# Optimization experiments

Measured on AMD Instinct MI355X. Metric: run time of the kernel, lower is better.

The kernel has to match this reference:

```python
import jax, jax.numpy as jnp
import numpy as np

# Sizes (match input_specs)
B = 50                 # number of CRN graphs in the batch
NS_PER, NR_PER = 2000, 4000
N_S, N_R = B * NS_PER, B * NR_PER   # 100k species, 200k reactions total
E = 1_000_000          # bipartite edges
D = 128                # d_model
L = 2                  # n_layers
N_TYPES, P_DIM = 16, 8
MAX_SPECIES_IDX = 2000


def setup_inputs() -> dict:
    key = jax.random.key(0)
    ks = jax.random.split(key, 12)
    inp = {
        "species_indices": jax.random.randint(ks[0], (N_S,), 0, MAX_SPECIES_IDX, dtype=jnp.int32),
        "is_external": jax.random.randint(ks[1], (N_S,), 0, 2, dtype=jnp.int32),
        "propensity_type_ids": jax.random.randint(ks[2], (N_R,), 0, N_TYPES, dtype=jnp.int32),
        "propensity_params": jax.random.normal(ks[3], (N_R, P_DIM), dtype=jnp.float32),
        "edge_species": jax.random.randint(ks[4], (E,), 0, N_S, dtype=jnp.int32),
        "edge_reaction": jax.random.randint(ks[5], (E,), 0, N_R, dtype=jnp.int32),
        # contiguous per-graph segment ids (graphs are equal-sized)
        "species_batch": jnp.repeat(jnp.arange(B, dtype=jnp.int32), NS_PER),
        "reaction_batch": jnp.repeat(jnp.arange(B, dtype=jnp.int32), NR_PER),
        # learned parameters
        "species_table": jax.random.normal(ks[6], (MAX_SPECIES_IDX, D), dtype=jnp.float32) * 0.02,
        "external_table": jax.random.normal(ks[7], (2, D), dtype=jnp.float32) * 0.02,
        "type_table": jax.random.normal(ks[8], (N_TYPES, D), dtype=jnp.float32) * 0.02,
        "W_param": jax.random.normal(ks[9], (P_DIM, D), dtype=jnp.float32) * 0.1,
        "b_param": jnp.zeros((D,), dtype=jnp.float32),
        # per-layer message-passing weights: concat([h, msg]) -> d
        "Wr": jax.random.normal(ks[10], (L, 2 * D, D), dtype=jnp.float32) * 0.05,
        "br": jnp.zeros((L, D), dtype=jnp.float32),
        "Ws": jax.random.normal(ks[11], (L, 2 * D, D), dtype=jnp.float32) * 0.05,
        "bs": jnp.zeros((L, D), dtype=jnp.float32),
    }
    return inp


def reference(species_indices, is_external, propensity_type_ids, propensity_params,
              edge_species, edge_reaction, species_batch, reaction_batch,
              species_table, external_table, type_table, W_param, b_param,
              Wr, br, Ws, bs):
    # Initial embeddings
    h_s = species_table[species_indices] + external_table[is_external]          # (N_S, D)
    h_r = type_table[propensity_type_ids] + propensity_params @ W_param + b_param  # (N_R, D)

    n_s, n_r = h_s.shape[0], h_r.shape[0]
    # Alternating bipartite sum message passing (SumMessagePassingLayer)
    for l in range(Wr.shape[0]):
        m_r = jax.ops.segment_sum(h_s[edge_species], edge_reaction, num_segments=n_r)
        h_r = jax.nn.relu(jnp.concatenate([h_r, m_r], axis=-1) @ Wr[l] + br[l])
        m_s = jax.ops.segment_sum(h_r[edge_reaction], edge_species, num_segments=n_s)
        h_s = jax.nn.relu(jnp.concatenate([h_s, m_s], axis=-1) @ Ws[l] + bs[l])

    # Segment-mean pooling per graph (index_add then divide by counts)
    pooled_s = jax.ops.segment_sum(h_s, species_batch, num_segments=B) / float(NS_PER)
    pooled_r = jax.ops.segment_sum(h_r, reaction_batch, num_segments=B) / float(NR_PER)
    context = jnp.concatenate([pooled_s, pooled_r], axis=-1)  # (B, 2D); dropout p=0 -> identity
    return context
```

## Files before the change

kernel.cpp:

```cpp
#include <hip/hip_runtime.h>
#include <stdint.h>

#define NS 100000
#define NR 200000
#define EE 1000000
#define DD 128
#define NB 50
#define NSP 2000
#define NRP 4000
#define BSH 10
#define NBR 196
#define NBS 98
#define CHUNK 8192

typedef short bf16x8 __attribute__((ext_vector_type(8)));
typedef float f32x4 __attribute__((ext_vector_type(4)));
typedef unsigned u32x4 __attribute__((ext_vector_type(4)));

__device__ __forceinline__ unsigned short f2bf(float f){
  unsigned u = __float_as_uint(f);
  u = (u + 0x7FFFu + ((u >> 16) & 1u)) >> 16;
  return (unsigned short)u;
}
__device__ __forceinline__ float bf2f(unsigned short s){
  return __uint_as_float(((unsigned)s) << 16);
}
__device__ __forceinline__ unsigned packbf(float a, float b){
  return (unsigned)f2bf(a) | ((unsigned)f2bf(b) << 16);
}
__device__ __forceinline__ float bflo(unsigned p){ return __uint_as_float(p << 16); }
__device__ __forceinline__ float bfhi(unsigned p){ return __uint_as_float(p & 0xFFFF0000u); }

__global__ void pack_w(const float* __restrict__ Wr, const float* __restrict__ Ws,
                       unsigned short* __restrict__ Wp){
  int g = blockIdx.x*256 + threadIdx.x;
  if (g >= 4*32768) return;
  int j = g & 7; int rest = g >> 3;
  int lane = rest & 63; rest >>= 6;
  int ks = rest & 7; rest >>= 3;
  int ct = rest & 7; int mat = rest >> 3;
  int k  = ks*32 + (lane >> 4)*8 + j;
  int cc = ct*16 + (lane & 15);
  const float* src = (mat < 2) ? (Wr + (size_t)mat*256*DD) : (Ws + (size_t)(mat-2)*256*DD);
  Wp[g] = f2bf(src[(size_t)k*DD + cc]);
}

__global__ __launch_bounds__(256) void init_all(const int* __restrict__ si, const int* __restrict__ ext,
        const int* __restrict__ tid, const float* __restrict__ pp,
        const float* __restrict__ st, const float* __restrict__ et, const float* __restrict__ tt,
        const float* __restrict__ Wpar, const float* __restrict__ bpar,
        unsigned short* __restrict__ hs, unsigned short* __restrict__ hr){
  int g = blockIdx.x*256 + threadIdx.x;
  int row = g >> 4, colb = (g & 15) * 8;
  if (row < NS){
    const float* a = st + (size_t)si[row]*DD + colb;
    const float* b = et + (size_t)ext[row]*DD + colb;
    float4 x0 = ((const float4*)a)[0], x1 = ((const float4*)a)[1];
    float4 y0 = ((const float4*)b)[0], y1 = ((const float4*)b)[1];
    u32x4 o;
    o.x = packbf(x0.x+y0.x, x0.y+y0.y);
    o.y = packbf(x0.z+y0.z, x0.w+y0.w);
    o.z = packbf(x1.x+y1.x, x1.y+y1.y);
    o.w = packbf(x1.z+y1.z, x1.w+y1.w);
    *(u32x4*)(hs + (size_t)row*DD + colb) = o;
  } else {
    int r = row - NS;
    const float* tb = tt + (size_t)tid[r]*DD + colb;
    float4 a0 = ((const float4*)tb)[0], a1 = ((const float4*)tb)[1];
    float4 b0 = ((const float4*)(bpar+colb))[0], b1 = ((const float4*)(bpar+colb))[1];
    a0.x += b0.x; a0.y += b0.y; a0.z += b0.z; a0.w += b0.w;
    a1.x += b1.x; a1.y += b1.y; a1.z += b1.z; a1.w += b1.w;
    const float* pr = pp + (size_t)r*8;
    float4 p0 = ((const float4*)pr)[0], p1 = ((const float4*)pr)[1];
    float w[8] = {p0.x,p0.y,p0.z,p0.w,p1.x,p1.y,p1.z,p1.w};
    #pragma unroll
    for (int p = 0; p < 8; p++){
      float4 w0 = ((const float4*)(Wpar + p*DD + colb))[0];
      float4 w1 = ((const float4*)(Wpar + p*DD + colb))[1];
      a0.x += w[p]*w0.x; a0.y += w[p]*w0.y; a0.z += w[p]*w0.z; a0.w += w[p]*w0.w;
      a1.x += w[p]*w1.x; a1.y += w[p]*w1.y; a1.z += w[p]*w1.z; a1.w += w[p]*w1.w;
    }
    u32x4 o;
    o.x = packbf(a0.x, a0.y); o.y = packbf(a0.z, a0.w);
    o.z = packbf(a1.x, a1.y); o.w = packbf(a1.z, a1.w);
    *(u32x4*)(hr + (size_t)r*DD + colb) = o;
  }
}

__global__ __launch_bounds__(256) void bucket_hist(const int* __restrict__ er, const int* __restrict__ es,
                                                   int* __restrict__ gcnt){
  __shared__ int cnt[NBR + NBS];
  int t = threadIdx.x;
  for (int j = t; j < NBR + NBS; j += 256) cnt[j] = 0;
  __syncthreads();
  long i0 = (long)blockIdx.x * 2048;
  for (int j = t; j < 2048; j += 256){
    long i = i0 + j;
    if (i < EE){
      atomicAdd(&cnt[er[i] >> BSH], 1);
      atomicAdd(&cnt[NBR + (es[i] >> BSH)], 1);
    }
  }
  __syncthreads();
  for (int j = t; j < NBR + NBS; j += 256)
    if (cnt[j]) atomicAdd(&gcnt[j], cnt[j]);
}

__global__ __launch_bounds__(256) void bucket_scan(const int* __restrict__ gcnt,
        int* __restrict__ bktOffR, int* __restrict__ bktOffS,
        int* __restrict__ gCurR, int* __restrict__ gCurS){
  __shared__ int a[256];
  int t = threadIdx.x;
  int own = (t < NBR) ? gcnt[t] : 0;
  a[t] = own; __syncthreads();
  for (int d = 1; d < 256; d <<= 1){
    int x = (t >= d) ? a[t-d] : 0;
    __syncthreads(); a[t] += x; __syncthreads();
  }
  if (t < NBR){ int v = a[t] - own; bktOffR[t] = v; gCurR[t] = v; }
  if (t == 0) bktOffR[NBR] = EE;
  __syncthreads();
  own = (t < NBS) ? gcnt[NBR + t] : 0;
  a[t] = own; __syncthreads();
  for (int d = 1; d < 256; d <<= 1){
    int x = (t >= d) ? a[t-d] : 0;
    __syncthreads(); a[t] += x; __syncthreads();
  }
  if (t < NBS){ int v = a[t] - own; bktOffS[t] = v; gCurS[t] = v; }
  if (t == 0) bktOffS[NBS] = EE;
}

__global__ __launch_bounds__(256) void bin_edges(const int* __restrict__ er, const int* __restrict__ es,
        int* __restrict__ gCurR, int* __restrict__ gCurS,
        unsigned* __restrict__ recR, unsigned* __restrict__ recS){
  __shared__ unsigned stage[CHUNK];
  __shared__ unsigned char stageb[CHUNK];
  __shared__ int cnt[256], scn[256], pref[256], gbase[256], lcur[256];
  int t = threadIdx.x;
  int side = blockIdx.y;
  const int* dest = side ? es : er;
  const int* srca = side ? er : es;
  int* gCur = side ? gCurS : gCurR;
  unsigned* rec = side ? recS : recR;
  int nbkt = side ? NBS : NBR;
  long i0 = (long)blockIdx.x * CHUNK;
  int n = (EE - i0 < CHUNK) ? (int)(EE - i0) : CHUNK;
  cnt[t] = 0;
  __syncthreads();
  for (int j = t; j < n; j += 256)
    atomicAdd(&cnt[dest[i0 + j] >> BSH], 1);
  __syncthreads();
  scn[t] = cnt[t];
  __syncthreads();
  for (int d = 1; d < 256; d <<= 1){
    int x = (t >= d) ? scn[t-d] : 0;
    __syncthreads(); scn[t] += x; __syncthreads();
  }
  pref[t] = scn[t] - cnt[t];
  lcur[t] = scn[t] - cnt[t];
  if (t < nbkt && cnt[t] > 0) gbase[t] = atomicAdd(&gCur[t], cnt[t]);
  __syncthreads();
  for (int j = t; j < n; j += 256){
    int d = dest[i0 + j];
    int s = srca[i0 + j];
    int b = d >> BSH;
    int p = atomicAdd(&lcur[b], 1);
    stage[p] = ((unsigned)(d - (b << BSH)) << 18) | (unsigned)s;
    stageb[p] = (unsigned char)b;
  }
  __syncthreads();
  for (int e = t; e < n; e += 256){
    int b = stageb[e];
    rec[gbase[b] + (e - pref[b])] = stage[e];
  }
}

__global__ __launch_bounds__(256) void build_csr(const unsigned* __restrict__ recR, const unsigned* __restrict__ recS,
        const int* __restrict__ bktOffR, const int* __restrict__ bktOffS,
        int* __restrict__ csrR, int* __restrict__ csrS,
        int* __restrict__ offsR, int* __restrict__ offsS){
  __shared__ int hist[1024], pref[1024], cur[1024], ws[256];
  int t = threadIdx.x;
  int bb = blockIdx.x;
  const unsigned* rec; const int* bktOff; int* csr; int* offs; int N;
  if (bb < NBR){ rec = recR; bktOff = bktOffR; csr = csrR; offs = offsR; N = NR; }
  else { bb -= NBR; rec = recS; bktOff = bktOffS; csr = csrS; offs = offsS; N = NS; }
  int d0 = bb << BSH;
  int base = bktOff[bb], cnt_ = bktOff[bb+1] - base;
  #pragma unroll
  for (int j = 0; j < 4; j++) hist[t*4+j] = 0;
  __syncthreads();
  for (int e = t; e < cnt_; e += 256)
    atomicAdd(&hist[rec[base + e] >> 18], 1);
  __syncthreads();
  int s = 0, h[4];
  #pragma unroll
  for (int j = 0; j < 4; j++){ h[j] = hist[t*4+j]; s += h[j]; }
  ws[t] = s;
  __syncthreads();
  for (int d = 1; d < 256; d <<= 1){
    int x = (t >= d) ? ws[t-d] : 0;
    __syncthreads(); ws[t] += x; __syncthreads();
  }
  int run = ws[t] - s;
  #pragma unroll
  for (int j = 0; j < 4; j++){ pref[t*4+j] = run; cur[t*4+j] = base + run; run += h[j]; }
  __syncthreads();
  int DPB = N - d0; if (DPB > 1024) DPB = 1024;
  #pragma unroll
  for (int j = 0; j < 4; j++){
    int i = t*4 + j;
    if (i < DPB) offs[d0 + i] = base + pref[i];
  }
  if (t == 0 && d0 + DPB == N) offs[N] = EE;
  __syncthreads();
  for (int e = t; e < cnt_; e += 256){
    unsigned r = rec[base + e];
    int pos = atomicAdd(&cur[r >> 18], 1);
    csr[pos] = (int)(r & 0x3FFFFu);
  }
}

__global__ __launch_bounds__(256) void gather(const unsigned short* __restrict__ h, const int* __restrict__ offs,
        const int* __restrict__ csr, unsigned short* __restrict__ m, int nrows){
  int gw = (blockIdx.x * 256 + threadIdx.x) >> 6;
  int lane = threadIdx.x & 63;
  int quad = lane >> 4, sub = lane & 15;
  int r = gw*4 + quad;
  if (r >= nrows) return;
  int b = offs[r], e = offs[r+1];
  float a0=0,a1=0,a2=0,a3=0,a4=0,a5=0,a6=0,a7=0;
  float c0=0,c1=0,c2=0,c3=0,c4=0,c5=0,c6=0,c7=0;
  int k = b;
  for (; k + 2 <= e; k += 2){
    int s0 = csr[k], s1 = csr[k+1];
    u32x4 p = *(const u32x4*)(h + (size_t)s0*DD + sub*8);
    u32x4 q = *(const u32x4*)(h + (size_t)s1*DD + sub*8);
    a0 += bflo(p.x); a1 += bfhi(p.x); a2 += bflo(p.y); a3 += bfhi(p.y);
    a4 += bflo(p.z); a5 += bfhi(p.z); a6 += bflo(p.w); a7 += bfhi(p.w);
    c0 += bflo(q.x); c1 += bfhi(q.x); c2 += bflo(q.y); c3 += bfhi(q.y);
    c4 += bflo(q.z); c5 += bfhi(q.z); c6 += bflo(q.w); c7 += bfhi(q.w);
  }
  if (k < e){
    u32x4 p = *(const u32x4*)(h + (size_t)csr[k]*DD + sub*8);
    a0 += bflo(p.x); a1 += bfhi(p.x); a2 += bflo(p.y); a3 += bfhi(p.y);
    a4 += bflo(p.z); a5 += bfhi(p.z); a6 += bflo(p.w); a7 += bfhi(p.w);
  }
  u32x4 o;
  o.x = packbf(a0+c0, a1+c1); o.y = packbf(a2+c2, a3+c3);
  o.z = packbf(a4+c4, a5+c5); o.w = packbf(a6+c6, a7+c7);
  *(u32x4*)(m + (size_t)r*DD + sub*8) = o;
}

__global__ __launch_bounds__(256) void relu_gemm(const unsigned short* __restrict__ H,
        const unsigned short* __restrict__ M, const unsigned short* __restrict__ Wp,
        const float* __restrict__ bias, unsigned short* __restrict__ Hout, int N)
{
  int t = threadIdx.x;
  int lane = t & 63;
  int w = t >> 6;
  int rlo = lane & 15, quad = lane >> 4;
  int ct0 = w * 2;

  bf16x8 bf[16];
  #pragma unroll
  for (int ks = 0; ks < 8; ks++){
    bf[ks*2+0] = *(const bf16x8*)(Wp + (size_t)(((ct0+0)*8 + ks)*64 + lane) * 8);
    bf[ks*2+1] = *(const bf16x8*)(Wp + (size_t)(((ct0+1)*8 + ks)*64 + lane) * 8);
  }
  float bv0 = bias[(ct0+0)*16 + rlo];
  float bv1 = bias[(ct0+1)*16 + rlo];

  int ntiles = N >> 5;
  for (int tile = blockIdx.x; tile < ntiles; tile += gridDim.x){
    int row0 = tile * 32;
    f32x4 acc[2][2];
    #pragma unroll
    for (int i = 0; i < 2; i++)
      #pragma unroll
      for (int j = 0; j < 2; j++){ f32x4 z = {0.f,0.f,0.f,0.f}; acc[i][j] = z; }

    #pragma unroll
    for (int ks = 0; ks < 8; ks++){
      const unsigned short* src = (ks < 4) ? H : M;
      int kloc = (ks & 3) * 32 + quad * 8;
      bf16x8 a0 = *(const bf16x8*)(src + (size_t)(row0 + rlo) * DD + kloc);
      bf16x8 a1 = *(const bf16x8*)(src + (size_t)(row0 + 16 + rlo) * DD + kloc);
      acc[0][0] = __builtin_amdgcn_mfma_f32_16x16x32_bf16(a0, bf[ks*2+0], acc[0][0], 0, 0, 0);
      acc[0][1] = __builtin_amdgcn_mfma_f32_16x16x32_bf16(a0, bf[ks*2+1], acc[0][1], 0, 0, 0);
      acc[1][0] = __builtin_amdgcn_mfma_f32_16x16x32_bf16(a1, bf[ks*2+0], acc[1][0], 0, 0, 0);
      acc[1][1] = __builtin_amdgcn_mfma_f32_16x16x32_bf16(a1, bf[ks*2+1], acc[1][1], 0, 0, 0);
    }

    #pragma unroll
    for (int rb = 0; rb < 2; rb++){
      #pragma unroll
      for (int i = 0; i < 4; i++){
        int row = row0 + rb*16 + quad*4 + i;
        float v0 = acc[rb][0][i] + bv0;
        float v1 = acc[rb][1][i] + bv1;
        v0 = v0 > 0.f ? v0 : 0.f;
        v1 = v1 > 0.f ? v1 : 0.f;
        Hout[(size_t)row*DD + (ct0+0)*16 + rlo] = f2bf(v0);
        Hout[(size_t)row*DD + (ct0+1)*16 + rlo] = f2bf(v1);
      }
    }
  }
}

__global__ __launch_bounds__(256) void pool(const unsigned short* __restrict__ hs,
        const unsigned short* __restrict__ hr, float* __restrict__ out){
  __shared__ float red[16][128];
  int b = blockIdx.x, part = blockIdx.y;
  int t = threadIdx.x;
  int rg = t >> 4, sub = t & 15;
  const unsigned short* src; int row0, outoff; float scale;
  if (part < 4){ src = hs; row0 = b*NSP + part*500; outoff = b*256; scale = 1.f/NSP; }
  else { src = hr; row0 = b*NRP + (part-4)*500; outoff = b*256 + 128; scale = 1.f/NRP; }
  float a0=0,a1=0,a2=0,a3=0,a4=0,a5=0,a6=0,a7=0;
  for (int r = rg; r < 500; r += 16){
    u32x4 p = *(const u32x4*)(src + (size_t)(row0+r)*DD + sub*8);
    a0 += bflo(p.x); a1 += bfhi(p.x);
    a2 += bflo(p.y); a3 += bfhi(p.y);
    a4 += bflo(p.z); a5 += bfhi(p.z);
    a6 += bflo(p.w); a7 += bfhi(p.w);
  }
  float* rr = &red[rg][sub*8];
  rr[0]=a0; rr[1]=a1; rr[2]=a2; rr[3]=a3; rr[4]=a4; rr[5]=a5; rr[6]=a6; rr[7]=a7;
  __syncthreads();
  if (t < 128){
    float s = 0.f;
    #pragma unroll
    for (int g = 0; g < 16; g++) s += red[g][t];
    atomicAdd(&out[outoff + t], s * scale);
  }
}

extern "C" void kernel_launch(void* const* d_in, const int* in_sizes, int n_in,
                              void* d_out, int out_size, void* d_ws, size_t ws_size,
                              hipStream_t stream)
{
  const int*   si   = (const int*)d_in[0];
  const int*   ext  = (const int*)d_in[1];
  const int*   tid  = (const int*)d_in[2];
  const float* pp   = (const float*)d_in[3];
  const int*   es   = (const int*)d_in[4];
  const int*   er   = (const int*)d_in[5];
  const float* st   = (const float*)d_in[8];
  const float* et   = (const float*)d_in[9];
  const float* tt   = (const float*)d_in[10];
  const float* Wpar = (const float*)d_in[11];
  const float* bpar = (const float*)d_in[12];
  const float* Wr   = (const float*)d_in[13];
  const float* br   = (const float*)d_in[14];
  const float* Ws   = (const float*)d_in[15];
  const float* bs   = (const float*)d_in[16];
  float* out = (float*)d_out;

  char* basep = (char*)d_ws; size_t off = 0;
  auto alloc = [&](size_t bytes)->char*{
    char* r = basep + off; off = (off + bytes + 255) & ~(size_t)255; return r;
  };
  unsigned short* h_s = (unsigned short*)alloc((size_t)NS*DD*2);
  unsigned short* h_r = (unsigned short*)alloc((size_t)NR*DD*2);
  unsigned short* msg = (unsigned short*)alloc((size_t)NR*DD*2);
  unsigned short* Wp  = (unsigned short*)alloc((size_t)4*32768*2);
  int* offsR = (int*)alloc((size_t)(NR+1)*4);
  int* offsS = (int*)alloc((size_t)(NS+1)*4);
  int* csrR  = (int*)alloc((size_t)EE*4);
  int* csrS  = (int*)alloc((size_t)EE*4);
  unsigned* recR = (unsigned*)alloc((size_t)EE*4);
  unsigned* recS = (unsigned*)alloc((size_t)EE*4);
  int* gcnt   = (int*)alloc(2048);
  int* bktOffR= (int*)alloc(2048);
  int* bktOffS= (int*)alloc(2048);
  int* gCurR  = (int*)alloc(2048);
  int* gCurS  = (int*)alloc(2048);

  hipMemsetAsync(gcnt, 0, 2048, stream);
  hipMemsetAsync(d_out, 0, (size_t)out_size*4, stream);

  pack_w<<<512, 256, 0, stream>>>(Wr, Ws, Wp);
  init_all<<<(NS+NR)*16/256, 256, 0, stream>>>(si, ext, tid, pp, st, et, tt, Wpar, bpar, h_s, h_r);

  bucket_hist<<<(EE + 2047)/2048, 256, 0, stream>>>(er, es, gcnt);
  bucket_scan<<<1, 256, 0, stream>>>(gcnt, bktOffR, bktOffS, gCurR, gCurS);
  bin_edges<<<dim3((EE + CHUNK - 1)/CHUNK, 2), 256, 0, stream>>>(er, es, gCurR, gCurS, recR, recS);
  build_csr<<<NBR + NBS, 256, 0, stream>>>(recR, recS, bktOffR, bktOffS, csrR, csrS, offsR, offsS);

  for (int l = 0; l < 2; l++){
    gather<<<(NR + 15)/16, 256, 0, stream>>>(h_s, offsR, csrR, msg, NR);
    relu_gemm<<<1024, 256, 0, stream>>>(h_r, msg, Wp + (size_t)l*32768, br + (size_t)l*DD, h_r, NR);
    gather<<<(NS + 15)/16, 256, 0, stream>>>(h_r, offsS, csrS, msg, NS);
    relu_gemm<<<1024, 256, 0, stream>>>(h_s, msg, Wp + (size_t)(2+l)*32768, bs + (size_t)l*DD, h_s, NS);
  }

  pool<<<dim3(NB, 12), 256, 0, stream>>>(h_s, h_r, out);
}
```

Measured before the change: 550.5 us.

## Fuse neighbor gather into ReLU GEMM per 32-row tile via shared memory

```diff
diff --git a/kernel.cpp b/kernel.cpp
--- a/kernel.cpp
+++ b/kernel.cpp
@@ -16,6 +16,7 @@
 typedef short bf16x8 __attribute__((ext_vector_type(8)));
 typedef float f32x4 __attribute__((ext_vector_type(4)));
 typedef unsigned u32x4 __attribute__((ext_vector_type(4)));
+typedef unsigned u32x2 __attribute__((ext_vector_type(2)));
 
 __device__ __forceinline__ unsigned short f2bf(float f){
   unsigned u = __float_as_uint(f);
@@ -30,6 +31,11 @@
 }
 __device__ __forceinline__ float bflo(unsigned p){ return __uint_as_float(p << 16); }
 __device__ __forceinline__ float bfhi(unsigned p){ return __uint_as_float(p & 0xFFFF0000u); }
+
+__device__ __forceinline__ void acc8(float* a, u32x4 p){
+  a[0] += bflo(p.x); a[1] += bfhi(p.x); a[2] += bflo(p.y); a[3] += bfhi(p.y);
+  a[4] += bflo(p.z); a[5] += bfhi(p.z); a[6] += bflo(p.w); a[7] += bfhi(p.w);
+}
 
 __global__ void pack_w(const float* __restrict__ Wr, const float* __restrict__ Ws,
                        unsigned short* __restrict__ Wp){
@@ -221,89 +227,122 @@
   }
 }
 
-__global__ __launch_bounds__(256) void gather(const unsigned short* __restrict__ h, const int* __restrict__ offs,
-        const int* __restrict__ csr, unsigned short* __restrict__ m, int nrows){
-  int gw = (blockIdx.x * 256 + threadIdx.x) >> 6;
-  int lane = threadIdx.x & 63;
-  int quad = lane >> 4, sub = lane & 15;
-  int r = gw*4 + quad;
-  if (r >= nrows) return;
-  int b = offs[r], e = offs[r+1];
-  float a0=0,a1=0,a2=0,a3=0,a4=0,a5=0,a6=0,a7=0;
-  float c0=0,c1=0,c2=0,c3=0,c4=0,c5=0,c6=0,c7=0;
-  int k = b;
-  for (; k + 2 <= e; k += 2){
-    int s0 = csr[k], s1 = csr[k+1];
-    u32x4 p = *(const u32x4*)(h + (size_t)s0*DD + sub*8);
-    u32x4 q = *(const u32x4*)(h + (size_t)s1*DD + sub*8);
-    a0 += bflo(p.x); a1 += bfhi(p.x); a2 += bflo(p.y); a3 += bfhi(p.y);
-    a4 += bflo(p.z); a5 += bfhi(p.z); a6 += bflo(p.w); a7 += bfhi(p.w);
-    c0 += bflo(q.x); c1 += bfhi(q.x); c2 += bflo(q.y); c3 += bfhi(q.y);
-    c4 += bflo(q.z); c5 += bfhi(q.z); c6 += bflo(q.w); c7 += bfhi(q.w);
-  }
-  if (k < e){
-    u32x4 p = *(const u32x4*)(h + (size_t)csr[k]*DD + sub*8);
-    a0 += bflo(p.x); a1 += bfhi(p.x); a2 += bflo(p.y); a3 += bfhi(p.y);
-    a4 += bflo(p.z); a5 += bfhi(p.z); a6 += bflo(p.w); a7 += bfhi(p.w);
-  }
-  u32x4 o;
-  o.x = packbf(a0+c0, a1+c1); o.y = packbf(a2+c2, a3+c3);
-  o.z = packbf(a4+c4, a5+c5); o.w = packbf(a6+c6, a7+c7);
-  *(u32x4*)(m + (size_t)r*DD + sub*8) = o;
-}
-
-__global__ __launch_bounds__(256) void relu_gemm(const unsigned short* __restrict__ H,
-        const unsigned short* __restrict__ M, const unsigned short* __restrict__ Wp,
-        const float* __restrict__ bias, unsigned short* __restrict__ Hout, int N)
+__global__ __launch_bounds__(256) void fused_layer(
+        const unsigned short* __restrict__ gsrc,
+        const unsigned short* __restrict__ hself,
+        const int* __restrict__ offs, const int* __restrict__ csr,
+        const unsigned short* __restrict__ Wp, const float* __restrict__ bias,
+        unsigned short* __restrict__ hout)
 {
+  __shared__ unsigned short msgT[32*DD];
   int t = threadIdx.x;
   int lane = t & 63;
   int w = t >> 6;
-  int rlo = lane & 15, quad = lane >> 4;
+  int quad = lane >> 4, rlo = lane & 15;
+  int row0 = blockIdx.x * 32;
+
+  {
+    int lr1 = w*8 + quad, lr2 = lr1 + 4;
+    int r1 = row0 + lr1, r2 = row0 + lr2;
+    int k1 = offs[r1], e1 = offs[r1+1];
+    int k2 = offs[r2], e2 = offs[r2+1];
+    float xa[8] = {0,0,0,0,0,0,0,0};
+    float ya[8] = {0,0,0,0,0,0,0,0};
+    while (k1 + 2 <= e1 && k2 + 2 <= e2){
+      int sA = csr[k1], sB = csr[k1+1], sC = csr[k2], sD = csr[k2+1];
+      u32x4 pA = *(const u32x4*)(gsrc + (size_t)sA*DD + rlo*8);
+      u32x4 pB = *(const u32x4*)(gsrc + (size_t)sB*DD + rlo*8);
+      u32x4 pC = *(const u32x4*)(gsrc + (size_t)sC*DD + rlo*8);
+      u32x4 pD = *(const u32x4*)(gsrc + (size_t)sD*DD + rlo*8);
+      acc8(xa, pA); acc8(xa, pB); acc8(ya, pC); acc8(ya, pD);
+      k1 += 2; k2 += 2;
+    }
+    while (k1 + 2 <= e1){
+      int sA = csr[k1], sB = csr[k1+1];
+      u32x4 pA = *(const u32x4*)(gsrc + (size_t)sA*DD + rlo*8);
+      u32x4 pB = *(const u32x4*)(gsrc + (size_t)sB*DD + rlo*8);
+      acc8(xa, pA); acc8(xa, pB);
+      k1 += 2;
+    }
+    while (k2 + 2 <= e2){
+      int sC = csr[k2], sD = csr[k2+1];
+      u32x4 pC = *(const u32x4*)(gsrc + (size_t)sC*DD + rlo*8);
+      u32x4 pD = *(const u32x4*)(gsrc + (size_t)sD*DD + rlo*8);
+      acc8(ya, pC); acc8(ya, pD);
+      k2 += 2;
+    }
+    if (k1 < e1){ u32x4 p = *(const u32x4*)(gsrc + (size_t)csr[k1]*DD + rlo*8); acc8(xa, p); }
+    if (k2 < e2){ u32x4 p = *(const u32x4*)(gsrc + (size_t)csr[k2]*DD + rlo*8); acc8(ya, p); }
+    u32x4 o1, o2;
+    o1.x = packbf(xa[0],xa[1]); o1.y = packbf(xa[2],xa[3]);
+    o1.z = packbf(xa[4],xa[5]); o1.w = packbf(xa[6],xa[7]);
+    o2.x = packbf(ya[0],ya[1]); o2.y = packbf(ya[2],ya[3]);
+    o2.z = packbf(ya[4],ya[5]); o2.w = packbf(ya[6],ya[7]);
+    *(u32x4*)(msgT + lr1*DD + ((rlo ^ (lr1 & 7)) * 8)) = o1;
+    *(u32x4*)(msgT + lr2*DD + ((rlo ^ (lr2 & 7)) * 8)) = o2;
+  }
+  __syncthreads();
+
   int ct0 = w * 2;
-
-  bf16x8 bf[16];
+  bf16x8 wf[16];
   #pragma unroll
   for (int ks = 0; ks < 8; ks++){
-    bf[ks*2+0] = *(const bf16x8*)(Wp + (size_t)(((ct0+0)*8 + ks)*64 + lane) * 8);
-    bf[ks*2+1] = *(const bf16x8*)(Wp + (size_t)(((ct0+1)*8 + ks)*64 + lane) * 8);
-  }
-  float bv0 = bias[(ct0+0)*16 + rlo];
-  float bv1 = bias[(ct0+1)*16 + rlo];
-
-  int ntiles = N >> 5;
-  for (int tile = blockIdx.x; tile < ntiles; tile += gridDim.x){
-    int row0 = tile * 32;
-    f32x4 acc[2][2];
+    wf[ks*2+0] = *(const bf16x8*)(Wp + (size_t)(((ct0+0)*8 + ks)*64 + lane) * 8);
+    wf[ks*2+1] = *(const bf16x8*)(Wp + (size_t)(((ct0+1)*8 + ks)*64 + lane) * 8);
+  }
+  bf16x8 Hb0[4], Hb1[4];
+  #pragma unroll
+  for (int ks = 0; ks < 4; ks++){
+    int kloc = ks*32 + quad*8;
+    Hb0[ks] = *(const bf16x8*)(hself + (size_t)(row0 + rlo) * DD + kloc);
+    Hb1[ks] = *(const bf16x8*)(hself + (size_t)(row0 + 16 + rlo) * DD + kloc);
+  }
+  bf16x8 Mb0[4], Mb1[4];
+  #pragma unroll
+  for (int ks2 = 0; ks2 < 4; ks2++){
+    int c8 = ks2*4 + quad;
+    int lr0 = rlo, lr1 = 16 + rlo;
+    Mb0[ks2] = *(const bf16x8*)(msgT + lr0*DD + ((c8 ^ (lr0 & 7)) * 8));
+    Mb1[ks2] = *(const bf16x8*)(msgT + lr1*DD + ((c8 ^ (lr1 & 7)) * 8));
+  }
+
+  f32x4 acc[2][2];
+  #pragma unroll
+  for (int i = 0; i < 2; i++)
     #pragma unroll
-    for (int i = 0; i < 2; i++)
-      #pragma unroll
-      for (int j = 0; j < 2; j++){ f32x4 z = {0.f,0.f,0.f,0.f}; acc[i][j] = z; }
-
-    #pragma unroll
-    for (int ks = 0; ks < 8; ks++){
-      const unsigned short* src = (ks < 4) ? H : M;
-      int kloc = (ks & 3) * 32 + quad * 8;
-      bf16x8 a0 = *(const bf16x8*)(src + (size_t)(row0 + rlo) * DD + kloc);
-      bf16x8 a1 = *(const bf16x8*)(src + (size_t)(row0 + 16 + rlo) * DD + kloc);
-      acc[0][0] = __builtin_amdgcn_mfma_f32_16x16x32_bf16(a0, bf[ks*2+0], acc[0][0], 0, 0, 0);
-      acc[0][1] = __builtin_amdgcn_mfma_f32_16x16x32_bf16(a0, bf[ks*2+1], acc[0][1], 0, 0, 0);
-      acc[1][0] = __builtin_amdgcn_mfma_f32_16x16x32_bf16(a1, bf[ks*2+0], acc[1][0], 0, 0, 0);
-      acc[1][1] = __builtin_amdgcn_mfma_f32_16x16x32_bf16(a1, bf[ks*2+1], acc[1][1], 0, 0, 0);
-    }
-
+    for (int j = 0; j < 2; j++){ f32x4 z = {0.f,0.f,0.f,0.f}; acc[i][j] = z; }
+
+  #pragma unroll
+  for (int ks = 0; ks < 4; ks++){
+    acc[0][0] = __builtin_amdgcn_mfma_f32_16x16x32_bf16(wf[ks*2+0], Hb0[ks], acc[0][0], 0, 0, 0);
+    acc[0][1] = __builtin_amdgcn_mfma_f32_16x16x32_bf16(wf[ks*2+1], Hb0[ks], acc[0][1], 0, 0, 0);
+    acc[1][0] = __builtin_amdgcn_mfma_f32_16x16x32_bf16(wf[ks*2+0], Hb1[ks], acc[1][0], 0, 0, 0);
+    acc[1][1] = __builtin_amdgcn_mfma_f32_16x16x32_bf16(wf[ks*2+1], Hb1[ks], acc[1][1], 0, 0, 0);
+  }
+  #pragma unroll
+  for (int ks2 = 0; ks2 < 4; ks2++){
+    int ks = 4 + ks2;
+    acc[0][0] = __builtin_amdgcn_mfma_f32_16x16x32_bf16(wf[ks*2+0], Mb0[ks2], acc[0][0], 0, 0, 0);
+    acc[0][1] = __builtin_amdgcn_mfma_f32_16x16x32_bf16(wf[ks*2+1], Mb0[ks2], acc[0][1], 0, 0, 0);
+    acc[1][0] = __builtin_amdgcn_mfma_f32_16x16x32_bf16(wf[ks*2+0], Mb1[ks2], acc[1][0], 0, 0, 0);
+    acc[1][1] = __builtin_amdgcn_mfma_f32_16x16x32_bf16(wf[ks*2+1], Mb1[ks2], acc[1][1], 0, 0, 0);
+  }
+
+  #pragma unroll
+  for (int c = 0; c < 2; c++){
+    float4 bv = *(const float4*)(bias + (ct0+c)*16 + quad*4);
     #pragma unroll
     for (int rb = 0; rb < 2; rb++){
-      #pragma unroll
-      for (int i = 0; i < 4; i++){
-        int row = row0 + rb*16 + quad*4 + i;
-        float v0 = acc[rb][0][i] + bv0;
-        float v1 = acc[rb][1][i] + bv1;
-        v0 = v0 > 0.f ? v0 : 0.f;
-        v1 = v1 > 0.f ? v1 : 0.f;
-        Hout[(size_t)row*DD + (ct0+0)*16 + rlo] = f2bf(v0);
-        Hout[(size_t)row*DD + (ct0+1)*16 + rlo] = f2bf(v1);
-      }
+      float v0 = acc[rb][c][0] + bv.x;
+      float v1 = acc[rb][c][1] + bv.y;
+      float v2 = acc[rb][c][2] + bv.z;
+      float v3 = acc[rb][c][3] + bv.w;
+      v0 = v0 > 0.f ? v0 : 0.f;
+      v1 = v1 > 0.f ? v1 : 0.f;
+      v2 = v2 > 0.f ? v2 : 0.f;
+      v3 = v3 > 0.f ? v3 : 0.f;
+      u32x2 o; o.x = packbf(v0, v1); o.y = packbf(v2, v3);
+      *(u32x2*)(hout + (size_t)(row0 + rb*16 + rlo)*DD + (ct0+c)*16 + quad*4) = o;
     }
   }
 }
@@ -361,39 +400,38 @@
   auto alloc = [&](size_t bytes)->char*{
     char* r = basep + off; off = (off + bytes + 255) & ~(size_t)255; return r;
   };
-  unsigned short* h_s = (unsigned short*)alloc((size_t)NS*DD*2);
-  unsigned short* h_r = (unsigned short*)alloc((size_t)NR*DD*2);
-  unsigned short* msg = (unsigned short*)alloc((size_t)NR*DD*2);
+  unsigned short* hs0 = (unsigned short*)alloc((size_t)NS*DD*2);
+  unsigned short* hs1 = (unsigned short*)alloc((size_t)NS*DD*2);
+  unsigned short* hr0 = (unsigned short*)alloc((size_t)NR*DD*2);
+  unsigned short* hr1 = (unsigned short*)alloc((size_t)NR*DD*2);
   unsigned short* Wp  = (unsigned short*)alloc((size_t)4*32768*2);
   int* offsR = (int*)alloc((size_t)(NR+1)*4);
   int* offsS = (int*)alloc((size_t)(NS+1)*4);
   int* csrR  = (int*)alloc((size_t)EE*4);
   int* csrS  = (int*)alloc((size_t)EE*4);
-  unsigned* recR = (unsigned*)alloc((size_t)EE*4);
-  unsigned* recS = (unsigned*)alloc((size_t)EE*4);
   int* gcnt   = (int*)alloc(2048);
   int* bktOffR= (int*)alloc(2048);
   int* bktOffS= (int*)alloc(2048);
   int* gCurR  = (int*)alloc(2048);
   int* gCurS  = (int*)alloc(2048);
+  unsigned* recR = (unsigned*)hs1;
+  unsigned* recS = (unsigned*)hr1;
 
   hipMemsetAsync(gcnt, 0, 2048, stream);
   hipMemsetAsync(d_out, 0, (size_t)out_size*4, stream);
 
   pack_w<<<512, 256, 0, stream>>>(Wr, Ws, Wp);
-  init_all<<<(NS+NR)*16/256, 256, 0, stream>>>(si, ext, tid, pp, st, et, tt, Wpar, bpar, h_s, h_r);
+  init_all<<<(NS+NR)*16/256, 256, 0, stream>>>(si, ext, tid, pp, st, et, tt, Wpar, bpar, hs0, hr0);
 
   bucket_hist<<<(EE + 2047)/2048, 256, 0, stream>>>(er, es, gcnt);
   bucket_scan<<<1, 256, 0, stream>>>(gcnt, bktOffR, bktOffS, gCurR, gCurS);
   bin_edges<<<dim3((EE + CHUNK - 1)/CHUNK, 2), 256, 0, stream>>>(er, es, gCurR, gCurS, recR, recS);
   build_csr<<<NBR + NBS, 256, 0, stream>>>(recR, recS, bktOffR, bktOffS, csrR, csrS, offsR, offsS);
 
-  for (int l = 0; l < 2; l++){
-    gather<<<(NR + 15)/16, 256, 0, stream>>>(h_s, offsR, csrR, msg, NR);
-    relu_gemm<<<1024, 256, 0, stream>>>(h_r, msg, Wp + (size_t)l*32768, br + (size_t)l*DD, h_r, NR);
-    gather<<<(NS + 15)/16, 256, 0, stream>>>(h_r, offsS, csrS, msg, NS);
-    relu_gemm<<<1024, 256, 0, stream>>>(h_s, msg, Wp + (size_t)(2+l)*32768, bs + (size_t)l*DD, h_s, NS);
-  }
-
-  pool<<<dim3(NB, 12), 256, 0, stream>>>(h_s, h_r, out);
-}
+  fused_layer<<<NR/32, 256, 0, stream>>>(hs0, hr0, offsR, csrR, Wp + (size_t)0*32768, br + (size_t)0*DD, hr1);
+  fused_layer<<<NS/32, 256, 0, stream>>>(hr1, hs0, offsS, csrS, Wp + (size_t)2*32768, bs + (size_t)0*DD, hs1);
+  fused_layer<<<NR/32, 256, 0, stream>>>(hs1, hr1, offsR, csrR, Wp + (size_t)1*32768, br + (size_t)1*DD, hr0);
+  fused_layer<<<NS/32, 256, 0, stream>>>(hr0, hs1, offsS, csrS, Wp + (size_t)3*32768, bs + (size_t)1*DD, hs0);
+
+  pool<<<dim3(NB, 12), 256, 0, stream>>>(hs0, hr0, out);
+}
```

New measurement: 521.9 us. -5.2%, faster.
